# Performance work log

Hardware: AMD Instinct MI355X
Metric: run time of the kernel (lower is better)

## Reference

```python
import jax, jax.numpy as jnp
import numpy as np

N = 131072   # total nodes (B*C)
D = 128      # hidden_dim
H = 4        # gat_heads == hgt_heads
HD = 32      # head dim
T = 3        # number of edge types
E = 262144   # edges per edge type
B = 512      # graphs
EPS = 1e-6
SLOPE = 0.2  # LeakyReLU negative slope (module-wide and GAT internal)


def _rmsnorm(x, scale):
    return scale * x * jax.lax.rsqrt(jnp.mean(x * x, axis=-1, keepdims=True) + EPS)


def _gat(x, ei, W, a_src, a_dst, b):
    """HeteroConv(sum) of per-edge-type GATConv (concat heads, self-loops)."""
    loops = jnp.arange(N)

    def one(ei_t, W_t, as_t, ad_t):
        h = (x @ W_t).reshape(N, H, HD)                         # [N,H,HD]
        src = jnp.concatenate([ei_t[0], loops])                 # add self loops
        dst = jnp.concatenate([ei_t[1], loops])
        a = jax.nn.leaky_relu((h * as_t).sum(-1)[src] + (h * ad_t).sum(-1)[dst], SLOPE)  # [E',H]
        m = jax.ops.segment_max(a, dst, num_segments=N)
        ex = jnp.exp(a - m[dst])
        s = jax.ops.segment_sum(ex, dst, num_segments=N)
        alpha = ex / s[dst]                                     # segment softmax per dst
        out = jax.ops.segment_sum(h[src] * alpha[..., None], dst, num_segments=N)
        return out.reshape(N, D)

    return jax.vmap(one)(ei, W, a_src, a_dst).sum(0) + b.sum(0)


def _hgt(x, ei, kw, kb, qw, qb, vw, vb, rel_k, rel_v, rel_p, aw, ab, skip):
    """HGTConv, single node type, T edge types; softmax over all incoming edges."""
    k = (x @ kw + kb).reshape(N, H, HD)
    q = (x @ qw + qb).reshape(N, H, HD)
    v = (x @ vw + vb).reshape(N, H, HD)
    kt = jnp.einsum('nhd,thde->tnhe', k, rel_k)                 # relation-specific keys
    vt = jnp.einsum('nhd,thde->tnhe', v, rel_v)
    k_msg = jax.vmap(lambda a, i: a[i])(kt, ei[:, 0]).reshape(T * E, H, HD)
    v_msg = jax.vmap(lambda a, i: a[i])(vt, ei[:, 0]).reshape(T * E, H, HD)
    dst = ei[:, 1].reshape(T * E)
    p = jnp.broadcast_to(rel_p[:, None, :], (T, E, H)).reshape(T * E, H)
    score = (q[dst] * k_msg).sum(-1) * p / np.sqrt(HD)          # [T*E,H]
    m = jax.ops.segment_max(score, dst, num_segments=N)
    ex = jnp.exp(score - m[dst])
    s = jax.ops.segment_sum(ex, dst, num_segments=N)
    alpha = ex / s[dst]
    out = jax.ops.segment_sum(alpha[..., None] * v_msg, dst, num_segments=N).reshape(N, D)
    out = jax.nn.gelu(out, approximate=False) @ aw + ab
    g = jax.nn.sigmoid(skip)
    return g * out + (1.0 - g) * x


def _res(x_old, x_new, scale):
    # norm -> (dropout is identity in eval) -> residual -> LeakyReLU(0.2)
    return jax.nn.leaky_relu(x_old + _rmsnorm(x_new, scale), SLOPE)


def setup_inputs() -> dict:
    key = jax.random.key(0)
    ks = iter(jax.random.split(key, 48))

    def nrm(shape, std=0.1):
        return jax.random.normal(next(ks), shape, jnp.float32) * std

    inp = {}
    inp['x_cell'] = nrm((N, D), 1.0)
    inp['x_cell_embedded'] = nrm((N, D), 1.0)
    inp['z_h'] = nrm((B, D), 1.0)
    inp['edge_index'] = jax.random.randint(next(ks), (T, 2, E), 0, N)
    for l in ('gat1', 'gat2'):
        inp[l + '_w'] = nrm((T, D, H * HD))
        inp[l + '_att_src'] = nrm((T, H, HD))
        inp[l + '_att_dst'] = nrm((T, H, HD))
        inp[l + '_b'] = jnp.zeros((T, D), jnp.float32)
    inp['norm1_s'] = jnp.ones((D,), jnp.float32)
    inp['norm2_s'] = jnp.ones((D,), jnp.float32)
    inp['norm3_s'] = jnp.ones((D,), jnp.float32)
    for nm in ('k', 'q', 'v'):
        inp['hgt_%s_w' % nm] = nrm((D, D))
        inp['hgt_%s_b' % nm] = jnp.zeros((D,), jnp.float32)
    inp['hgt_rel_k'] = nrm((T, H, HD, HD))
    inp['hgt_rel_v'] = nrm((T, H, HD, HD))
    inp['hgt_rel_p'] = jnp.ones((T, H), jnp.float32)
    inp['hgt_a_w'] = nrm((D, D))
    inp['hgt_a_b'] = jnp.zeros((D,), jnp.float32)
    inp['hgt_skip'] = jnp.ones((), jnp.float32)
    inp['inj_w'] = nrm((D, D))
    inp['inj_b'] = jnp.zeros((D,), jnp.float32)
    inp['film_w1'] = nrm((D, 2 * D))
    inp['film_b1'] = jnp.zeros((2 * D,), jnp.float32)
    inp['film_w2'] = nrm((2 * D, 2 * D), 0.001)
    inp['film_b2'] = jnp.zeros((2 * D,), jnp.float32)
    inp['batch_size'] = B
    return inp


def reference(x_cell, x_cell_embedded, z_h, edge_index,
              gat1_w, gat1_att_src, gat1_att_dst, gat1_b,
              gat2_w, gat2_att_src, gat2_att_dst, gat2_b,
              norm1_s, norm2_s, norm3_s,
              hgt_k_w, hgt_k_b, hgt_q_w, hgt_q_b, hgt_v_w, hgt_v_b,
              hgt_rel_k, hgt_rel_v, hgt_rel_p, hgt_a_w, hgt_a_b, hgt_skip,
              inj_w, inj_b, film_w1, film_b1, film_w2, film_b2, batch_size):
    x1 = _res(x_cell, _gat(x_cell, edge_index, gat1_w, gat1_att_src, gat1_att_dst, gat1_b), norm1_s)
    x2 = _res(x1, _gat(x1, edge_index, gat2_w, gat2_att_src, gat2_att_dst, gat2_b), norm2_s)
    x3 = _res(x2, _hgt(x2, edge_index, hgt_k_w, hgt_k_b, hgt_q_w, hgt_q_b, hgt_v_w, hgt_v_b,
                       hgt_rel_k, hgt_rel_v, hgt_rel_p, hgt_a_w, hgt_a_b, hgt_skip), norm3_s)
    x3 = x3 + x_cell_embedded @ inj_w + inj_b                   # input injection
    # FiLM (per-graph z, fixed batch mode)
    gb = jax.nn.gelu(z_h @ film_w1 + film_b1, approximate=False) @ film_w2 + film_b2
    gamma, beta = jnp.split(gb, 2, axis=-1)
    gamma = 0.1 * jnp.tanh(gamma)
    beta = 0.1 * jnp.tanh(beta)
    C = N // batch_size
    out = (1.0 + gamma)[:, None, :] * x3.reshape(batch_size, C, D) + beta[:, None, :]
    return out.reshape(N, D)
```

## Files before the change

### kernel.cpp

```cpp
#include <hip/hip_runtime.h>
#include <math.h>
#include <cstdint>

#define NN     131072
#define DDIM   128
#define NHEAD  4
#define HDIM   32
#define NTYPE  3
#define NEDGE  262144
#define NGRAPH 512
#define EPSV   1e-6f
#define SLOPEV 0.2f

typedef unsigned short bfraw;
typedef __attribute__((ext_vector_type(8))) short bf16x8;
typedef __attribute__((ext_vector_type(4))) float f32x4;

__device__ __forceinline__ float lrelu(float x){ return x >= 0.f ? x : SLOPEV*x; }
__device__ __forceinline__ float gelu_f(float x){ return 0.5f*x*(1.f+erff(x*0.70710678118654752f)); }
__device__ __forceinline__ bfraw f2bf(float f){
  unsigned int u = __float_as_uint(f);
  u += 0x7fffu + ((u >> 16) & 1u);
  return (bfraw)(u >> 16);
}
__device__ __forceinline__ float4 ld_bf4(const bfraw* p){
  uint2 u = *reinterpret_cast<const uint2*>(p);
  float4 r;
  r.x = __uint_as_float(u.x << 16); r.y = __uint_as_float(u.x & 0xffff0000u);
  r.z = __uint_as_float(u.y << 16); r.w = __uint_as_float(u.y & 0xffff0000u);
  return r;
}
__device__ __forceinline__ bf16x8 pack_bf8(const float* p){
  float4 u = *reinterpret_cast<const float4*>(p);
  float4 v = *reinterpret_cast<const float4*>(p+4);
  bf16x8 r;
  r[0]=(short)f2bf(u.x); r[1]=(short)f2bf(u.y); r[2]=(short)f2bf(u.z); r[3]=(short)f2bf(u.w);
  r[4]=(short)f2bf(v.x); r[5]=(short)f2bf(v.y); r[6]=(short)f2bf(v.z); r[7]=(short)f2bf(v.w);
  return r;
}

__global__ void fill_k(float* __restrict__ p, float v, int n){
  int i = blockIdx.x*blockDim.x + threadIdx.x;
  int stride = gridDim.x*blockDim.x;
  for (; i < n; i += stride) p[i] = v;
}

__global__ void conv_k(const float* __restrict__ in, bfraw* __restrict__ out, int n){
  int i = blockIdx.x*blockDim.x + threadIdx.x;
  int stride = gridDim.x*blockDim.x;
  for (; i < n; i += stride) out[i] = f2bf(in[i]);
}

__global__ void hist_k(const int* __restrict__ ei, int* __restrict__ deg){
  int idx = blockIdx.x*256 + threadIdx.x;
  int t = idx >> 18, e = idx & (NEDGE-1);
  int d = ei[(long)t*2*NEDGE + NEDGE + e];
  atomicAdd(&deg[t*NN + d], 1);
}

__global__ void scan_a_k(const int* __restrict__ deg, int* __restrict__ rp,
                         int* __restrict__ csum){
  __shared__ int sh[256];
  int t = blockIdx.y, chunk = blockIdx.x, tid = threadIdx.x;
  const int* dp = deg + (long)t*NN + chunk*2048 + tid*8;
  int v[8]; int s = 0;
  #pragma unroll
  for (int i=0;i<8;i++){ v[i] = dp[i]; s += v[i]; }
  sh[tid] = s; __syncthreads();
  for (int off=1; off<256; off<<=1){
    int x = (tid>=off) ? sh[tid-off] : 0;
    __syncthreads();
    sh[tid] += x;
    __syncthreads();
  }
  int run = sh[tid] - s;
  int* op = rp + (long)t*(NN+1) + chunk*2048 + tid*8;
  #pragma unroll
  for (int i=0;i<8;i++){ op[i] = run; run += v[i]; }
  if (tid == 255) csum[t*64 + chunk] = sh[255];
}

__global__ void scan_b_k(int* __restrict__ csum){
  __shared__ int sh[64];
  int t = blockIdx.x, tid = threadIdx.x;
  int s = csum[t*64 + tid];
  sh[tid] = s; __syncthreads();
  for (int off=1; off<64; off<<=1){
    int x = (tid>=off) ? sh[tid-off] : 0;
    __syncthreads();
    sh[tid] += x;
    __syncthreads();
  }
  csum[t*64 + tid] = sh[tid] - s;
}

__global__ void scan_c_k(int* __restrict__ rp, const int* __restrict__ csum){
  int t = blockIdx.y, chunk = blockIdx.x, tid = threadIdx.x;
  int add = csum[t*64 + chunk];
  int* op = rp + (long)t*(NN+1) + chunk*2048 + tid*8;
  #pragma unroll
  for (int i=0;i<8;i++) op[i] += add;
  if (chunk == 63 && tid == 255) rp[(long)t*(NN+1) + NN] = NEDGE;
}

__global__ void scatter_k(const int* __restrict__ ei, const int* __restrict__ rp,
                          int* __restrict__ cnt, int* __restrict__ srcs){
  int idx = blockIdx.x*256 + threadIdx.x;
  int t = idx >> 18, e = idx & (NEDGE-1);
  int s = ei[(long)t*2*NEDGE + e];
  int d = ei[(long)t*2*NEDGE + NEDGE + e];
  int pos = rp[(long)t*(NN+1) + d] + atomicAdd(&cnt[t*NN + d], 1);
  srcs[(long)t*NEDGE + pos] = s;
}

__global__ void wswz_k(const float* g0a, const float* g0b, const float* g0c,
                       const float* g1a, const float* g1b, const float* g1c,
                       const float* qw,
                       const float* wk, const float* wv,
                       const float* aw, const float* injw,
                       bfraw* __restrict__ Wall)
{
  int y = blockIdx.y;
  const float* src;
  switch(y){
    case 0: src = g0a; break;  case 1: src = g0b; break;  case 2: src = g0c; break;
    case 3: src = g1a; break;  case 4: src = g1b; break;  case 5: src = g1c; break;
    case 6: src = qw; break;
    case 7: case 8: case 9: src = wk + (long)(y-7)*16384; break;
    case 10: case 11: case 12: src = wv + (long)(y-10)*16384; break;
    case 13: src = aw; break;
    default: src = injw; break;
  }
  int i = blockIdx.x*256 + threadIdx.x;
  int j = i & 7, lane = (i>>3) & 63, kc = (i>>9) & 3, nt = i >> 11;
  int k = kc*32 + ((lane>>4)<<3) + j;
  int n = nt*16 + (lane & 15);
  Wall[(long)y*16384 + i] = f2bf(src[k*DDIM + n]);
}

__global__ void gatproj_k(const float* __restrict__ w, const float* __restrict__ asrc,
                          const float* __restrict__ adst, bfraw* __restrict__ out)
{
  int i = blockIdx.x*256 + threadIdx.x;
  int j = i & 7, lane = (i>>3) & 63, kc = (i>>9) & 3, nt = i >> 11;
  int k = kc*32 + ((lane>>4)<<3) + j;
  int n = nt*16 + (lane & 15);
  float s = 0.f;
  if (n < 24){
    int t = n >> 3, sd = (n >> 2) & 1, hh = n & 3;
    const float* a  = (sd ? adst : asrc) + ((long)t*NHEAD + hh)*HDIM;
    const float* wr = w + ((long)t*DDIM + k)*DDIM + hh*HDIM;
    #pragma unroll 8
    for (int dd=0; dd<HDIM; dd++) s += wr[dd]*a[dd];
  }
  out[i] = f2bf(s);
}

__device__ __forceinline__ void load_afrags_bf16(const bfraw* __restrict__ A,
    long blockRow, int tid, bf16x8 a0[4], bf16x8 a1[4])
{
  const int w = tid >> 6, lane = tid & 63;
  const long rowA = blockRow + w*32 + (lane & 15);
  const bfraw* A0 = A + rowA*DDIM + ((lane>>4)<<3);
  #pragma unroll
  for (int kc=0;kc<4;kc++){
    a0[kc] = *reinterpret_cast<const bf16x8*>(A0 + kc*32);
    a1[kc] = *reinterpret_cast<const bf16x8*>(A0 + 16*DDIM + kc*32);
  }
}

__device__ __forceinline__ void load_afrags_f32(const float* __restrict__ A,
    long blockRow, int tid, bf16x8 a0[4], bf16x8 a1[4])
{
  const int w = tid >> 6, lane = tid & 63;
  const long rowA = blockRow + w*32 + (lane & 15);
  const float* A0 = A + rowA*DDIM + ((lane>>4)<<3);
  #pragma unroll
  for (int kc=0;kc<4;kc++){
    a0[kc] = pack_bf8(A0 + kc*32);
    a1[kc] = pack_bf8(A0 + 16*DDIM + kc*32);
  }
}

__device__ __forceinline__ void mfma_128(const bfraw* Wl, int lane,
    bf16x8 a0[4], bf16x8 a1[4], f32x4 acc0[8], f32x4 acc1[8])
{
  const f32x4 zz = {0.f,0.f,0.f,0.f};
  #pragma unroll
  for (int nt=0;nt<8;nt++){ acc0[nt]=zz; acc1[nt]=zz; }
  #pragma unroll
  for (int nt=0;nt<8;nt++){
    #pragma unroll
    for (int kc=0;kc<4;kc++){
      bf16x8 b = *reinterpret_cast<const bf16x8*>(Wl + ((nt*4+kc)*64 + lane)*8);
      acc0[nt] = __builtin_amdgcn_mfma_f32_16x16x32_bf16(a0[kc], b, acc0[nt], 0, 0, 0);
      acc1[nt] = __builtin_amdgcn_mfma_f32_16x16x32_bf16(a1[kc], b, acc1[nt], 0, 0, 0);
    }
  }
}

__device__ __forceinline__ void gemm_store_bf16(f32x4 acc0[8], f32x4 acc1[8],
    const float* bias, bfraw* __restrict__ Cb, long blockRow, int tid)
{
  const int w = tid>>6, lane = tid&63, q = lane>>4;
  #pragma unroll
  for (int g=0; g<2; g++){
    #pragma unroll
    for (int nt=0;nt<8;nt++){
      int col = nt*16 + (lane & 15);
      float bv = bias ? bias[col] : 0.f;
      #pragma unroll
      for (int r=0;r<4;r++){
        long row = blockRow + w*32 + g*16 + q*4 + r;
        float v = (g ? acc1[nt][r] : acc0[nt][r]) + bv;
        Cb[row*DDIM + col] = f2bf(v);
      }
    }
  }
}

__global__ __launch_bounds__(256) void gemm_out_k(
    const bfraw* __restrict__ A, const bfraw* __restrict__ Wsw,
    const float* __restrict__ bias, bfraw* __restrict__ Cb)
{
  __shared__ bfraw Wl[16384];
  const int tid = threadIdx.x;
  const long blockRow = (long)blockIdx.x * 128;
  #pragma unroll
  for (int i=0;i<8;i++)
    *reinterpret_cast<uint4*>(Wl + (i*256+tid)*8) =
        *reinterpret_cast<const uint4*>(Wsw + (i*256+tid)*8);
  __syncthreads();
  bf16x8 a0[4], a1[4];
  load_afrags_bf16(A, blockRow, tid, a0, a1);
  f32x4 acc0[8], acc1[8];
  mfma_128(Wl, tid & 63, a0, a1, acc0, acc1);
  gemm_store_bf16(acc0, acc1, bias, Cb, blockRow, tid);
}

__global__ __launch_bounds__(256) void gemm3_k(
    const bfraw* __restrict__ A,
    const bfraw* __restrict__ W0, const bfraw* __restrict__ W1,
    const bfraw* __restrict__ W2,
    const float* __restrict__ b0, const float* __restrict__ b1,
    const float* __restrict__ b2,
    bfraw* __restrict__ O0, bfraw* __restrict__ O1, bfraw* __restrict__ O2,
    const bfraw* __restrict__ Psw, float* __restrict__ SS)
{
  __shared__ bfraw Wl[16384];
  const int tid = threadIdx.x;
  const long blockRow = (long)blockIdx.x * 128;
  const int w = tid >> 6, lane = tid & 63;
  bf16x8 a0[4], a1[4];
  load_afrags_bf16(A, blockRow, tid, a0, a1);
  const bfraw* Ws[3] = {W0, W1, W2};
  const float* bs[3] = {b0, b1, b2};
  bfraw* Os[3] = {O0, O1, O2};
  #pragma unroll
  for (int t=0;t<3;t++){
    __syncthreads();
    #pragma unroll
    for (int i=0;i<8;i++)
      *reinterpret_cast<uint4*>(Wl + (i*256+tid)*8) =
          *reinterpret_cast<const uint4*>(Ws[t] + (i*256+tid)*8);
    __syncthreads();
    f32x4 acc0[8], acc1[8];
    mfma_128(Wl, lane, a0, a1, acc0, acc1);
    gemm_store_bf16(acc0, acc1, bs[t], Os[t], blockRow, tid);
  }
  if (Psw){
    __syncthreads();
    #pragma unroll
    for (int i=0;i<2;i++)
      *reinterpret_cast<uint4*>(Wl + (i*256+tid)*8) =
          *reinterpret_cast<const uint4*>(Psw + (i*256+tid)*8);
    __syncthreads();
    const f32x4 zz = {0.f,0.f,0.f,0.f};
    f32x4 acc0[2], acc1[2];
    #pragma unroll
    for (int nt=0;nt<2;nt++){ acc0[nt]=zz; acc1[nt]=zz; }
    #pragma unroll
    for (int nt=0;nt<2;nt++){
      #pragma unroll
      for (int kc=0;kc<4;kc++){
        bf16x8 b = *reinterpret_cast<const bf16x8*>(Wl + ((nt*4+kc)*64 + lane)*8);
        acc0[nt] = __builtin_amdgcn_mfma_f32_16x16x32_bf16(a0[kc], b, acc0[nt], 0, 0, 0);
        acc1[nt] = __builtin_amdgcn_mfma_f32_16x16x32_bf16(a1[kc], b, acc1[nt], 0, 0, 0);
      }
    }
    const int q = lane >> 4;
    #pragma unroll
    for (int g=0; g<2; g++){
      #pragma unroll
      for (int nt=0;nt<2;nt++){
        int col = nt*16 + (lane & 15);
        if (col < 24){
          int tt = col >> 3, c = col & 7;
          #pragma unroll
          for (int r=0;r<4;r++){
            long row = blockRow + w*32 + g*16 + q*4 + r;
            SS[(((long)tt*NN + row)<<3) + c] = (g ? acc1[nt][r] : acc0[nt][r]);
          }
        }
      }
    }
  }
}

__global__ __launch_bounds__(256) void gemm_res3_k(
    const bfraw* __restrict__ A, const bfraw* __restrict__ Wsw,
    const float* __restrict__ bias, float* __restrict__ X,
    const float* __restrict__ norm, const float* __restrict__ skip)
{
  __shared__ bfraw Wl[16384];
  const int tid = threadIdx.x;
  const long blockRow = (long)blockIdx.x * 128;
  #pragma unroll
  for (int i=0;i<8;i++)
    *reinterpret_cast<uint4*>(Wl + (i*256+tid)*8) =
        *reinterpret_cast<const uint4*>(Wsw + (i*256+tid)*8);
  __syncthreads();
  bf16x8 a0[4], a1[4];
  load_afrags_bf16(A, blockRow, tid, a0, a1);
  f32x4 acc0[8], acc1[8];
  mfma_128(Wl, tid & 63, a0, a1, acc0, acc1);
  const int w = tid>>6, lane = tid&63, q = lane>>4;
  const float gsk = 1.f/(1.f + __expf(-skip[0]));
  #pragma unroll
  for (int g=0; g<2; g++){
    #pragma unroll
    for (int r=0;r<4;r++){
      long row = blockRow + w*32 + g*16 + q*4 + r;
      float vv[8], xx[8];
      float sq = 0.f;
      #pragma unroll
      for (int nt=0;nt<8;nt++){
        int col = nt*16 + (lane & 15);
        float o  = (g ? acc1[nt][r] : acc0[nt][r]) + bias[col];
        float xo = X[row*DDIM + col];
        float v  = gsk*o + (1.f-gsk)*xo;
        vv[nt] = v; xx[nt] = xo; sq += v*v;
      }
      sq += __shfl_xor(sq, 1, 64);
      sq += __shfl_xor(sq, 2, 64);
      sq += __shfl_xor(sq, 4, 64);
      sq += __shfl_xor(sq, 8, 64);
      float rr = rsqrtf(sq*(1.f/DDIM) + EPSV);
      #pragma unroll
      for (int nt=0;nt<8;nt++){
        int col = nt*16 + (lane & 15);
        X[row*DDIM + col] = lrelu(xx[nt] + norm[col]*vv[nt]*rr);
      }
    }
  }
}

__global__ __launch_bounds__(256) void gemm_film_k(
    const float* __restrict__ Af, const bfraw* __restrict__ Wsw,
    const float* __restrict__ bias, const float* __restrict__ Xadd,
    const float* __restrict__ gbt, float* __restrict__ out)
{
  __shared__ bfraw Wl[16384];
  const int tid = threadIdx.x;
  const long blockRow = (long)blockIdx.x * 128;
  #pragma unroll
  for (int i=0;i<8;i++)
    *reinterpret_cast<uint4*>(Wl + (i*256+tid)*8) =
        *reinterpret_cast<const uint4*>(Wsw + (i*256+tid)*8);
  __syncthreads();
  bf16x8 a0[4], a1[4];
  load_afrags_f32(Af, blockRow, tid, a0, a1);
  f32x4 acc0[8], acc1[8];
  mfma_128(Wl, tid & 63, a0, a1, acc0, acc1);
  const int w = tid>>6, lane = tid&63, q = lane>>4;
  #pragma unroll
  for (int g=0; g<2; g++){
    #pragma unroll
    for (int nt=0;nt<8;nt++){
      int col = nt*16 + (lane & 15);
      float bv = bias[col];
      #pragma unroll
      for (int r=0;r<4;r++){
        long row = blockRow + w*32 + g*16 + q*4 + r;
        long gi  = row >> 8;
        float v  = (g ? acc1[nt][r] : acc0[nt][r]) + bv + Xadd[row*DDIM + col];
        float ga = gbt[gi*256 + col];
        float be = gbt[gi*256 + 128 + col];
        out[row*DDIM + col] = (1.f + ga)*v + be;
      }
    }
  }
}

__global__ __launch_bounds__(256) void gat_fused_k(
    const int* __restrict__ rp, const int* __restrict__ srcs,
    const bfraw* __restrict__ H0, const bfraw* __restrict__ H1,
    const bfraw* __restrict__ H2, const float* __restrict__ SS,
    const float* __restrict__ gatb, const float* __restrict__ xold,
    const float* __restrict__ norm, float* __restrict__ X, bfraw* __restrict__ Xb)
{
  int node = blockIdx.x*8 + (threadIdx.x >> 5);
  int l = threadIdx.x & 31;
  int hd = l >> 3;
  const bfraw* Hs[3] = {H0, H1, H2};
  float tx=0.f, ty=0.f, tz=0.f, tw=0.f;
  #pragma unroll
  for (int t=0; t<3; t++){
    const bfraw* Ht = Hs[t];
    const float* St = SS + ((long)t*NN)*8;
    float dsv = St[(long)node*8 + 4 + hd];
    float e = __expf(lrelu(St[(long)node*8 + hd] + dsv));
    float lsum = e;
    float4 a4 = ld_bf4(Ht + (long)node*DDIM + l*4);
    a4.x *= e; a4.y *= e; a4.z *= e; a4.w *= e;
    int beg = rp[t*(NN+1) + node], end = rp[t*(NN+1) + node + 1];
    const int* sp = srcs + (long)t*NEDGE;
    for (int p=beg; p<end; p++){
      int s = sp[p];
      float ee = __expf(lrelu(St[(long)s*8 + hd] + dsv));
      float4 hv = ld_bf4(Ht + (long)s*DDIM + l*4);
      lsum += ee;
      a4.x += ee*hv.x; a4.y += ee*hv.y; a4.z += ee*hv.z; a4.w += ee*hv.w;
    }
    float inv = 1.f/lsum;
    tx += a4.x*inv; ty += a4.y*inv; tz += a4.z*inv; tw += a4.w*inv;
  }
  int f = l*4;
  tx += gatb[f]   + gatb[DDIM+f]   + gatb[2*DDIM+f];
  ty += gatb[f+1] + gatb[DDIM+f+1] + gatb[2*DDIM+f+1];
  tz += gatb[f+2] + gatb[DDIM+f+2] + gatb[2*DDIM+f+2];
  tw += gatb[f+3] + gatb[DDIM+f+3] + gatb[2*DDIM+f+3];
  float sq = tx*tx + ty*ty + tz*tz + tw*tw;
  sq += __shfl_xor(sq, 1, 64);
  sq += __shfl_xor(sq, 2, 64);
  sq += __shfl_xor(sq, 4, 64);
  sq += __shfl_xor(sq, 8, 64);
  sq += __shfl_xor(sq, 16, 64);
  float r = rsqrtf(sq*(1.f/DDIM) + EPSV);
  float4 x4 = *reinterpret_cast<const float4*>(xold + (long)node*DDIM + f);
  float4 o;
  o.x = lrelu(x4.x + norm[f]  *tx*r);
  o.y = lrelu(x4.y + norm[f+1]*ty*r);
  o.z = lrelu(x4.z + norm[f+2]*tz*r);
  o.w = lrelu(x4.w + norm[f+3]*tw*r);
  *reinterpret_cast<float4*>(X + (long)node*DDIM + f) = o;
  unsigned int lo = ((unsigned int)f2bf(o.y) << 16) | f2bf(o.x);
  unsigned int hi = ((unsigned int)f2bf(o.w) << 16) | f2bf(o.z);
  *reinterpret_cast<uint2*>(Xb + (long)node*DDIM + f) = make_uint2(lo, hi);
}

__global__ void fold_k(const float* __restrict__ w, const float* __restrict__ b,
                       const float* __restrict__ rel, float* __restrict__ Weff,
                       float* __restrict__ beff)
{
  int idx = blockIdx.x*256 + threadIdx.x;
  if (idx >= NTYPE*DDIM*DDIM) return;
  int he = idx & 127, c = (idx >> 7) & 127, t = idx >> 14;
  int h = he >> 5, e = he & 31;
  const float* wrow = w + (long)c*DDIM + h*HDIM;
  const float* relm = rel + ((long)(t*NHEAD + h)*HDIM)*HDIM + e;
  float s = 0.f;
  #pragma unroll 8
  for (int d=0; d<HDIM; d++) s += wrow[d] * relm[d*HDIM];
  Weff[(long)t*DDIM*DDIM + (long)c*DDIM + he] = s;
  if (c == 0){
    float sb = 0.f;
    #pragma unroll 8
    for (int d=0; d<HDIM; d++) sb += b[h*HDIM+d] * relm[d*HDIM];
    beff[(long)t*DDIM + he] = sb;
  }
}

__global__ __launch_bounds__(256) void hgt_score_pass_k(
    const int* __restrict__ rp, const int* __restrict__ srcs,
    const bfraw* __restrict__ qb, const bfraw* __restrict__ kt,
    const float* __restrict__ relp, float* __restrict__ E)
{
  int node = blockIdx.x*8 + (threadIdx.x >> 5);
  int l = threadIdx.x & 31;
  int hd = l >> 3, sub = l & 7;
  float4 qv = ld_bf4(qb + (long)node*DDIM + l*4);
  int beg = rp[node], end = rp[node+1];
  float scale = relp[hd] * 0.17677669529663687f;
  for (int p=beg; p<end; p++){
    int s = srcs[p];
    float4 kv = ld_bf4(kt + (long)s*DDIM + l*4);
    float dot = qv.x*kv.x + qv.y*kv.y + qv.z*kv.z + qv.w*kv.w;
    dot += __shfl_xor(dot, 1, 64);
    dot += __shfl_xor(dot, 2, 64);
    dot += __shfl_xor(dot, 4, 64);
    if (sub == 0) E[(long)p*4 + hd] = __expf(dot * scale);
  }
}

__global__ __launch_bounds__(256) void hgt_acc_fused_k(
    const int* __restrict__ rp, const int* __restrict__ srcs,
    const float* __restrict__ E, const bfraw* __restrict__ V0,
    const bfraw* __restrict__ V1, const bfraw* __restrict__ V2,
    bfraw* __restrict__ out)
{
  int node = blockIdx.x*8 + (threadIdx.x >> 5);
  int l = threadIdx.x & 31;
  int hd = l >> 3;
  float ax=0.f, ay=0.f, az=0.f, aw=0.f, lsum=0.f;
  const bfraw* Vs[3] = {V0, V1, V2};
  #pragma unroll
  for (int t=0; t<3; t++){
    const bfraw* Vt = Vs[t];
    const float* Ep = E + (long)t*NEDGE*4;
    const int* sp = srcs + (long)t*NEDGE;
    int beg = rp[t*(NN+1) + node], end = rp[t*(NN+1) + node + 1];
    for (int p=beg; p<end; p++){
      int s = sp[p];
      float ex = Ep[(long)p*4 + hd];
      float4 vv = ld_bf4(Vt + (long)s*DDIM + l*4);
      ax += ex*vv.x; ay += ex*vv.y; az += ex*vv.z; aw += ex*vv.w;
      lsum += ex;
    }
  }
  float inv = (lsum > 0.f) ? 1.f/lsum : 0.f;
  float o0 = gelu_f(ax*inv), o1 = gelu_f(ay*inv);
  float o2 = gelu_f(az*inv), o3 = gelu_f(aw*inv);
  unsigned int lo = ((unsigned int)f2bf(o1) << 16) | f2bf(o0);
  unsigned int hi = ((unsigned int)f2bf(o3) << 16) | f2bf(o2);
  *reinterpret_cast<uint2*>(out + (long)node*DDIM + l*4) = make_uint2(lo, hi);
}

__global__ void film1_k(const float* __restrict__ z, const float* __restrict__ w1,
                        const float* __restrict__ b1, float* __restrict__ f1)
{
  int idx = blockIdx.x*256 + threadIdx.x;
  if (idx >= NGRAPH*256) return;
  int j = idx & 255, b = idx >> 8;
  const float* zr = z + (long)b*DDIM;
  float s = b1[j];
  for (int k=0;k<DDIM;k++) s += zr[k] * w1[(long)k*256 + j];
  f1[idx] = gelu_f(s);
}

__global__ void film2_k(const float* __restrict__ f1, const float* __restrict__ w2,
                        const float* __restrict__ b2, float* __restrict__ gb)
{
  int idx = blockIdx.x*256 + threadIdx.x;
  if (idx >= NGRAPH*256) return;
  int j = idx & 255, b = idx >> 8;
  const float* fr = f1 + (long)b*256;
  float s = b2[j];
  for (int k=0;k<256;k++) s += fr[k] * w2[(long)k*256 + j];
  gb[idx] = 0.1f*tanhf(s);
}

extern "C" void kernel_launch(void* const* d_in, const int* in_sizes, int n_in,
                              void* d_out, int out_size, void* d_ws, size_t ws_size,
                              hipStream_t stream)
{
  (void)in_sizes; (void)n_in; (void)out_size; (void)ws_size;
  const float* x_cell = (const float*)d_in[0];
  const float* x_emb  = (const float*)d_in[1];
  const float* z_h    = (const float*)d_in[2];
  const int*   ei     = (const int*)d_in[3];
  const float* gw[2]  = {(const float*)d_in[4],  (const float*)d_in[8]};
  const float* gas[2] = {(const float*)d_in[5],  (const float*)d_in[9]};
  const float* gad[2] = {(const float*)d_in[6],  (const float*)d_in[10]};
  const float* gbi[2] = {(const float*)d_in[7],  (const float*)d_in[11]};
  const float* norm1  = (const float*)d_in[12];
  const float* norm2  = (const float*)d_in[13];
  const float* norm3  = (const float*)d_in[14];
  const float* kw = (const float*)d_in[15]; const float* kb = (const float*)d_in[16];
  const float* qw = (const float*)d_in[17]; const float* qb = (const float*)d_in[18];
  const float* vw = (const float*)d_in[19]; const float* vb = (const float*)d_in[20];
  const float* relk = (const float*)d_in[21];
  const float* relv = (const float*)d_in[22];
  const float* relp = (const float*)d_in[23];
  const float* aw = (const float*)d_in[24]; const float* ab = (const float*)d_in[25];
  const float* skip = (const float*)d_in[26];
  const float* injw = (const float*)d_in[27]; const float* injb = (const float*)d_in[28];
  const float* fw1 = (const float*)d_in[29]; const float* fb1 = (const float*)d_in[30];
  const float* fw2 = (const float*)d_in[31]; const float* fb2 = (const float*)d_in[32];

  const long ND = (long)NN*DDIM;
  float* X    = (float*)d_ws;
  float* K    = X + ND;
  bfraw* Xb   = (bfraw*)(K + ND);
  bfraw* Hb   = Xb + ND;
  float* Sbuf = (float*)(Hb + ND);
  float* sA   = Sbuf + (long)NTYPE*NEDGE*4;
  float* sB   = sA + (long)NN*4;
  float* WkE  = sB + (long)NN*4;
  float* bkE  = WkE + (long)NTYPE*DDIM*DDIM;
  float* WvE  = bkE + (long)NTYPE*DDIM;
  float* bvE  = WvE + (long)NTYPE*DDIM*DDIM;
  bfraw* Pswz = (bfraw*)(bvE + (long)NTYPE*DDIM);
  bfraw* Wall = Pswz + (long)2*4096;
  float* f1b  = (float*)(Wall + (long)15*16384);
  float* gbb  = f1b + (long)NGRAPH*256;
  int*   deg  = (int*)(gbb + (long)NGRAPH*256);
  int*   rp   = deg + (long)NTYPE*NN;
  int*   srcs = rp  + (long)NTYPE*(NN+1);
  int*   csum = srcs + (long)NTYPE*NEDGE;

  bfraw* Kb0 = (bfraw*)K;
  bfraw* Kb1 = Kb0 + ND;

  const dim3 b256(256);
  float* NF = nullptr;
  bfraw* NB = nullptr; (void)NB;

  fill_k<<<256, b256, 0, stream>>>((float*)deg, 0.f, NTYPE*NN);
  hist_k<<<(NTYPE*NEDGE)/256, b256, 0, stream>>>(ei, deg);
  scan_a_k<<<dim3(64, NTYPE), b256, 0, stream>>>(deg, rp, csum);
  scan_b_k<<<NTYPE, 64, 0, stream>>>(csum);
  scan_c_k<<<dim3(64, NTYPE), b256, 0, stream>>>(rp, csum);
  fill_k<<<256, b256, 0, stream>>>((float*)deg, 0.f, NTYPE*NN);
  scatter_k<<<(NTYPE*NEDGE)/256, b256, 0, stream>>>(ei, rp, deg, srcs);

  fold_k<<<(NTYPE*DDIM*DDIM)/256, b256, 0, stream>>>(kw, kb, relk, WkE, bkE);
  fold_k<<<(NTYPE*DDIM*DDIM)/256, b256, 0, stream>>>(vw, vb, relv, WvE, bvE);
  wswz_k<<<dim3(64, 15), b256, 0, stream>>>(
      gw[0], gw[0]+16384, gw[0]+32768,
      gw[1], gw[1]+16384, gw[1]+32768,
      qw, WkE, WvE, aw, injw, Wall);
  gatproj_k<<<16, b256, 0, stream>>>(gw[0], gas[0], gad[0], Pswz);
  gatproj_k<<<16, b256, 0, stream>>>(gw[1], gas[1], gad[1], Pswz + 4096);

  film1_k<<<(NGRAPH*256)/256, b256, 0, stream>>>(z_h, fw1, fb1, f1b);
  film2_k<<<(NGRAPH*256)/256, b256, 0, stream>>>(f1b, fw2, fb2, gbb);

  conv_k<<<2048, b256, 0, stream>>>(x_cell, Xb, (int)ND);
  for (int layer=0; layer<2; layer++){
    gemm3_k<<<NN/128, b256, 0, stream>>>(
        Xb,
        Wall + (long)(layer*3+0)*16384, Wall + (long)(layer*3+1)*16384,
        Wall + (long)(layer*3+2)*16384,
        NF, NF, NF,
        Hb, Kb0, Kb1,
        Pswz + (long)layer*4096, Sbuf);
    gat_fused_k<<<NN/8, b256, 0, stream>>>(
        rp, srcs, Hb, Kb0, Kb1, Sbuf, gbi[layer],
        (layer==0) ? x_cell : X, (layer==0) ? norm1 : norm2, X, Xb);
  }

  gemm3_k<<<NN/128, b256, 0, stream>>>(
      Xb, Wall + (long)6*16384, Wall + (long)7*16384, Wall + (long)8*16384,
      qb, bkE, bkE + DDIM,
      Kb0, Hb, Kb1, nullptr, nullptr);
  hgt_score_pass_k<<<NN/8, b256, 0, stream>>>(rp, srcs, Kb0, Hb, relp, Sbuf);
  hgt_score_pass_k<<<NN/8, b256, 0, stream>>>(rp + (NN+1), srcs + NEDGE, Kb0, Kb1,
      relp + NHEAD, Sbuf + (long)NEDGE*4);
  gemm_out_k<<<NN/128, b256, 0, stream>>>(Xb, Wall + (long)9*16384, bkE + 2*DDIM, Hb);
  hgt_score_pass_k<<<NN/8, b256, 0, stream>>>(rp + 2*(NN+1), srcs + 2*NEDGE, Kb0, Hb,
      relp + 2*NHEAD, Sbuf + (long)2*NEDGE*4);
  gemm3_k<<<NN/128, b256, 0, stream>>>(
      Xb, Wall + (long)10*16384, Wall + (long)11*16384, Wall + (long)12*16384,
      bvE, bvE + DDIM, bvE + 2*DDIM,
      Hb, Kb0, Kb1, nullptr, nullptr);
  hgt_acc_fused_k<<<NN/8, b256, 0, stream>>>(rp, srcs, Sbuf, Hb, Kb0, Kb1, Xb);
  gemm_res3_k<<<NN/128, b256, 0, stream>>>(Xb, Wall + (long)13*16384, ab,
                                           X, norm3, skip);
  gemm_film_k<<<NN/128, b256, 0, stream>>>(x_emb, Wall + (long)14*16384, injb,
                                           X, gbb, (float*)d_out);
}
```

Measured before the change: 962.6 us.

## Fuse conversion, HGT output+FiLM, score passes; fold rel_p scale; unroll edge loops

```diff
diff --git a/kernel.cpp b/kernel.cpp
--- a/kernel.cpp
+++ b/kernel.cpp
@@ -43,12 +43,6 @@
   int i = blockIdx.x*blockDim.x + threadIdx.x;
   int stride = gridDim.x*blockDim.x;
   for (; i < n; i += stride) p[i] = v;
-}
-
-__global__ void conv_k(const float* __restrict__ in, bfraw* __restrict__ out, int n){
-  int i = blockIdx.x*blockDim.x + threadIdx.x;
-  int stride = gridDim.x*blockDim.x;
-  for (; i < n; i += stride) out[i] = f2bf(in[i]);
 }
 
 __global__ void hist_k(const int* __restrict__ ei, int* __restrict__ deg){
@@ -239,7 +233,7 @@
 }
 
 __global__ __launch_bounds__(256) void gemm3_k(
-    const bfraw* __restrict__ A,
+    const bfraw* __restrict__ Ab, const float* __restrict__ Af,
     const bfraw* __restrict__ W0, const bfraw* __restrict__ W1,
     const bfraw* __restrict__ W2,
     const float* __restrict__ b0, const float* __restrict__ b1,
@@ -252,7 +246,8 @@
   const long blockRow = (long)blockIdx.x * 128;
   const int w = tid >> 6, lane = tid & 63;
   bf16x8 a0[4], a1[4];
-  load_afrags_bf16(A, blockRow, tid, a0, a1);
+  if (Af) load_afrags_f32(Af, blockRow, tid, a0, a1);
+  else    load_afrags_bf16(Ab, blockRow, tid, a0, a1);
   const bfraw* Ws[3] = {W0, W1, W2};
   const float* bs[3] = {b0, b1, b2};
   bfraw* Os[3] = {O0, O1, O2};
@@ -307,10 +302,13 @@
   }
 }
 
-__global__ __launch_bounds__(256) void gemm_res3_k(
-    const bfraw* __restrict__ A, const bfraw* __restrict__ Wsw,
-    const float* __restrict__ bias, float* __restrict__ X,
-    const float* __restrict__ norm, const float* __restrict__ skip)
+__global__ __launch_bounds__(256) void gemm_r3film_k(
+    const bfraw* __restrict__ Aattn, const bfraw* __restrict__ Waw,
+    const float* __restrict__ ab, const float* __restrict__ X,
+    const float* __restrict__ norm, const float* __restrict__ skip,
+    const float* __restrict__ xemb, const bfraw* __restrict__ Winj,
+    const float* __restrict__ injb, const float* __restrict__ gbt,
+    float* __restrict__ out)
 {
   __shared__ bfraw Wl[16384];
   const int tid = threadIdx.x;
@@ -318,12 +316,21 @@
   #pragma unroll
   for (int i=0;i<8;i++)
     *reinterpret_cast<uint4*>(Wl + (i*256+tid)*8) =
-        *reinterpret_cast<const uint4*>(Wsw + (i*256+tid)*8);
+        *reinterpret_cast<const uint4*>(Waw + (i*256+tid)*8);
   __syncthreads();
   bf16x8 a0[4], a1[4];
-  load_afrags_bf16(A, blockRow, tid, a0, a1);
-  f32x4 acc0[8], acc1[8];
-  mfma_128(Wl, tid & 63, a0, a1, acc0, acc1);
+  load_afrags_bf16(Aattn, blockRow, tid, a0, a1);
+  f32x4 accA0[8], accA1[8];
+  mfma_128(Wl, tid & 63, a0, a1, accA0, accA1);
+  __syncthreads();
+  #pragma unroll
+  for (int i=0;i<8;i++)
+    *reinterpret_cast<uint4*>(Wl + (i*256+tid)*8) =
+        *reinterpret_cast<const uint4*>(Winj + (i*256+tid)*8);
+  __syncthreads();
+  load_afrags_f32(xemb, blockRow, tid, a0, a1);
+  f32x4 accB0[8], accB1[8];
+  mfma_128(Wl, tid & 63, a0, a1, accB0, accB1);
   const int w = tid>>6, lane = tid&63, q = lane>>4;
   const float gsk = 1.f/(1.f + __expf(-skip[0]));
   #pragma unroll
@@ -336,9 +343,9 @@
       #pragma unroll
       for (int nt=0;nt<8;nt++){
         int col = nt*16 + (lane & 15);
-        float o  = (g ? acc1[nt][r] : acc0[nt][r]) + bias[col];
+        float oA = (g ? accA1[nt][r] : accA0[nt][r]) + ab[col];
         float xo = X[row*DDIM + col];
-        float v  = gsk*o + (1.f-gsk)*xo;
+        float v  = gsk*oA + (1.f-gsk)*xo;
         vv[nt] = v; xx[nt] = xo; sq += v*v;
       }
       sq += __shfl_xor(sq, 1, 64);
@@ -346,47 +353,13 @@
       sq += __shfl_xor(sq, 4, 64);
       sq += __shfl_xor(sq, 8, 64);
       float rr = rsqrtf(sq*(1.f/DDIM) + EPSV);
+      long gi = row >> 8;
       #pragma unroll
       for (int nt=0;nt<8;nt++){
         int col = nt*16 + (lane & 15);
-        X[row*DDIM + col] = lrelu(xx[nt] + norm[col]*vv[nt]*rr);
-      }
-    }
-  }
-}
-
-__global__ __launch_bounds__(256) void gemm_film_k(
-    const float* __restrict__ Af, const bfraw* __restrict__ Wsw,
-    const float* __restrict__ bias, const float* __restrict__ Xadd,
-    const float* __restrict__ gbt, float* __restrict__ out)
-{
-  __shared__ bfraw Wl[16384];
-  const int tid = threadIdx.x;
-  const long blockRow = (long)blockIdx.x * 128;
-  #pragma unroll
-  for (int i=0;i<8;i++)
-    *reinterpret_cast<uint4*>(Wl + (i*256+tid)*8) =
-        *reinterpret_cast<const uint4*>(Wsw + (i*256+tid)*8);
-  __syncthreads();
-  bf16x8 a0[4], a1[4];
-  load_afrags_f32(Af, blockRow, tid, a0, a1);
-  f32x4 acc0[8], acc1[8];
-  mfma_128(Wl, tid & 63, a0, a1, acc0, acc1);
-  const int w = tid>>6, lane = tid&63, q = lane>>4;
-  #pragma unroll
-  for (int g=0; g<2; g++){
-    #pragma unroll
-    for (int nt=0;nt<8;nt++){
-      int col = nt*16 + (lane & 15);
-      float bv = bias[col];
-      #pragma unroll
-      for (int r=0;r<4;r++){
-        long row = blockRow + w*32 + g*16 + q*4 + r;
-        long gi  = row >> 8;
-        float v  = (g ? acc1[nt][r] : acc0[nt][r]) + bv + Xadd[row*DDIM + col];
-        float ga = gbt[gi*256 + col];
-        float be = gbt[gi*256 + 128 + col];
-        out[row*DDIM + col] = (1.f + ga)*v + be;
+        float x3 = lrelu(xx[nt] + norm[col]*vv[nt]*rr);
+        float vB = (g ? accB1[nt][r] : accB0[nt][r]) + injb[col] + x3;
+        out[row*DDIM + col] = (1.f + gbt[gi*256 + col])*vB + gbt[gi*256 + 128 + col];
       }
     }
   }
@@ -403,27 +376,50 @@
   int l = threadIdx.x & 31;
   int hd = l >> 3;
   const bfraw* Hs[3] = {H0, H1, H2};
+  float dsv[3], ssl[3]; float4 hsl[3]; int beg[3], end[3];
+  #pragma unroll
+  for (int t=0; t<3; t++){
+    const float* St = SS + ((long)t*NN)*8;
+    dsv[t] = St[(long)node*8 + 4 + hd];
+    ssl[t] = St[(long)node*8 + hd];
+    hsl[t] = ld_bf4(Hs[t] + (long)node*DDIM + l*4);
+    beg[t] = rp[t*(NN+1) + node];
+    end[t] = rp[t*(NN+1) + node + 1];
+  }
   float tx=0.f, ty=0.f, tz=0.f, tw=0.f;
   #pragma unroll
   for (int t=0; t<3; t++){
     const bfraw* Ht = Hs[t];
     const float* St = SS + ((long)t*NN)*8;
-    float dsv = St[(long)node*8 + 4 + hd];
-    float e = __expf(lrelu(St[(long)node*8 + hd] + dsv));
-    float lsum = e;
-    float4 a4 = ld_bf4(Ht + (long)node*DDIM + l*4);
-    a4.x *= e; a4.y *= e; a4.z *= e; a4.w *= e;
-    int beg = rp[t*(NN+1) + node], end = rp[t*(NN+1) + node + 1];
     const int* sp = srcs + (long)t*NEDGE;
-    for (int p=beg; p<end; p++){
-      int s = sp[p];
-      float ee = __expf(lrelu(St[(long)s*8 + hd] + dsv));
-      float4 hv = ld_bf4(Ht + (long)s*DDIM + l*4);
-      lsum += ee;
-      a4.x += ee*hv.x; a4.y += ee*hv.y; a4.z += ee*hv.z; a4.w += ee*hv.w;
-    }
-    float inv = 1.f/lsum;
-    tx += a4.x*inv; ty += a4.y*inv; tz += a4.z*inv; tw += a4.w*inv;
+    const float d = dsv[t];
+    float e = __expf(lrelu(ssl[t] + d));
+    float lA = e, lB = 0.f;
+    float4 aA = make_float4(e*hsl[t].x, e*hsl[t].y, e*hsl[t].z, e*hsl[t].w);
+    float4 aB = make_float4(0.f,0.f,0.f,0.f);
+    int p = beg[t];
+    for (; p+1 < end[t]; p += 2){
+      int s0 = sp[p], s1 = sp[p+1];
+      float v0 = St[(long)s0*8 + hd];
+      float v1 = St[(long)s1*8 + hd];
+      float4 h0 = ld_bf4(Ht + (long)s0*DDIM + l*4);
+      float4 h1 = ld_bf4(Ht + (long)s1*DDIM + l*4);
+      float e0 = __expf(lrelu(v0 + d));
+      float e1 = __expf(lrelu(v1 + d));
+      lA += e0; lB += e1;
+      aA.x += e0*h0.x; aA.y += e0*h0.y; aA.z += e0*h0.z; aA.w += e0*h0.w;
+      aB.x += e1*h1.x; aB.y += e1*h1.y; aB.z += e1*h1.z; aB.w += e1*h1.w;
+    }
+    if (p < end[t]){
+      int s0 = sp[p];
+      float e0 = __expf(lrelu(St[(long)s0*8 + hd] + d));
+      float4 h0 = ld_bf4(Ht + (long)s0*DDIM + l*4);
+      lA += e0;
+      aA.x += e0*h0.x; aA.y += e0*h0.y; aA.z += e0*h0.z; aA.w += e0*h0.w;
+    }
+    float inv = 1.f/(lA + lB);
+    tx += (aA.x+aB.x)*inv; ty += (aA.y+aB.y)*inv;
+    tz += (aA.z+aB.z)*inv; tw += (aA.w+aB.w)*inv;
   }
   int f = l*4;
   tx += gatb[f]   + gatb[DDIM+f]   + gatb[2*DDIM+f];
@@ -450,46 +446,103 @@
 }
 
 __global__ void fold_k(const float* __restrict__ w, const float* __restrict__ b,
-                       const float* __restrict__ rel, float* __restrict__ Weff,
-                       float* __restrict__ beff)
+                       const float* __restrict__ rel, const float* __restrict__ scl,
+                       float* __restrict__ Weff, float* __restrict__ beff)
 {
   int idx = blockIdx.x*256 + threadIdx.x;
   if (idx >= NTYPE*DDIM*DDIM) return;
   int he = idx & 127, c = (idx >> 7) & 127, t = idx >> 14;
   int h = he >> 5, e = he & 31;
+  float fs = scl ? scl[t*NHEAD + h]*0.17677669529663687f : 1.f;
   const float* wrow = w + (long)c*DDIM + h*HDIM;
   const float* relm = rel + ((long)(t*NHEAD + h)*HDIM)*HDIM + e;
   float s = 0.f;
   #pragma unroll 8
   for (int d=0; d<HDIM; d++) s += wrow[d] * relm[d*HDIM];
-  Weff[(long)t*DDIM*DDIM + (long)c*DDIM + he] = s;
+  Weff[(long)t*DDIM*DDIM + (long)c*DDIM + he] = s*fs;
   if (c == 0){
     float sb = 0.f;
     #pragma unroll 8
     for (int d=0; d<HDIM; d++) sb += b[h*HDIM+d] * relm[d*HDIM];
-    beff[(long)t*DDIM + he] = sb;
-  }
-}
-
-__global__ __launch_bounds__(256) void hgt_score_pass_k(
+    beff[(long)t*DDIM + he] = sb*fs;
+  }
+}
+
+__global__ __launch_bounds__(256) void hgt_score2_k(
+    const int* __restrict__ rp, const int* __restrict__ srcs,
+    const bfraw* __restrict__ qb, const bfraw* __restrict__ kt0,
+    const bfraw* __restrict__ kt1, float* __restrict__ E)
+{
+  int node = blockIdx.x*8 + (threadIdx.x >> 5);
+  int l = threadIdx.x & 31;
+  int hd = l >> 3, sub = l & 7;
+  float4 qv = ld_bf4(qb + (long)node*DDIM + l*4);
+  #pragma unroll
+  for (int t=0; t<2; t++){
+    const bfraw* kt = t ? kt1 : kt0;
+    const int* sp = srcs + (long)t*NEDGE;
+    float* Et = E + (long)t*NEDGE*4;
+    int beg = rp[t*(NN+1) + node], end = rp[t*(NN+1) + node + 1];
+    int p = beg;
+    for (; p+1 < end; p += 2){
+      int s0 = sp[p], s1 = sp[p+1];
+      float4 k0 = ld_bf4(kt + (long)s0*DDIM + l*4);
+      float4 k1 = ld_bf4(kt + (long)s1*DDIM + l*4);
+      float d0 = qv.x*k0.x + qv.y*k0.y + qv.z*k0.z + qv.w*k0.w;
+      float d1 = qv.x*k1.x + qv.y*k1.y + qv.z*k1.z + qv.w*k1.w;
+      d0 += __shfl_xor(d0, 1, 64);  d1 += __shfl_xor(d1, 1, 64);
+      d0 += __shfl_xor(d0, 2, 64);  d1 += __shfl_xor(d1, 2, 64);
+      d0 += __shfl_xor(d0, 4, 64);  d1 += __shfl_xor(d1, 4, 64);
+      if (sub == 0){
+        Et[(long)p*4 + hd]     = __expf(d0);
+        Et[(long)(p+1)*4 + hd] = __expf(d1);
+      }
+    }
+    if (p < end){
+      int s0 = sp[p];
+      float4 k0 = ld_bf4(kt + (long)s0*DDIM + l*4);
+      float d0 = qv.x*k0.x + qv.y*k0.y + qv.z*k0.z + qv.w*k0.w;
+      d0 += __shfl_xor(d0, 1, 64);
+      d0 += __shfl_xor(d0, 2, 64);
+      d0 += __shfl_xor(d0, 4, 64);
+      if (sub == 0) Et[(long)p*4 + hd] = __expf(d0);
+    }
+  }
+}
+
+__global__ __launch_bounds__(256) void hgt_score1_k(
     const int* __restrict__ rp, const int* __restrict__ srcs,
     const bfraw* __restrict__ qb, const bfraw* __restrict__ kt,
-    const float* __restrict__ relp, float* __restrict__ E)
+    float* __restrict__ E)
 {
   int node = blockIdx.x*8 + (threadIdx.x >> 5);
   int l = threadIdx.x & 31;
   int hd = l >> 3, sub = l & 7;
   float4 qv = ld_bf4(qb + (long)node*DDIM + l*4);
   int beg = rp[node], end = rp[node+1];
-  float scale = relp[hd] * 0.17677669529663687f;
-  for (int p=beg; p<end; p++){
-    int s = srcs[p];
-    float4 kv = ld_bf4(kt + (long)s*DDIM + l*4);
-    float dot = qv.x*kv.x + qv.y*kv.y + qv.z*kv.z + qv.w*kv.w;
-    dot += __shfl_xor(dot, 1, 64);
-    dot += __shfl_xor(dot, 2, 64);
-    dot += __shfl_xor(dot, 4, 64);
-    if (sub == 0) E[(long)p*4 + hd] = __expf(dot * scale);
+  int p = beg;
+  for (; p+1 < end; p += 2){
+    int s0 = srcs[p], s1 = srcs[p+1];
+    float4 k0 = ld_bf4(kt + (long)s0*DDIM + l*4);
+    float4 k1 = ld_bf4(kt + (long)s1*DDIM + l*4);
+    float d0 = qv.x*k0.x + qv.y*k0.y + qv.z*k0.z + qv.w*k0.w;
+    float d1 = qv.x*k1.x + qv.y*k1.y + qv.z*k1.z + qv.w*k1.w;
+    d0 += __shfl_xor(d0, 1, 64);  d1 += __shfl_xor(d1, 1, 64);
+    d0 += __shfl_xor(d0, 2, 64);  d1 += __shfl_xor(d1, 2, 64);
+    d0 += __shfl_xor(d0, 4, 64);  d1 += __shfl_xor(d1, 4, 64);
+    if (sub == 0){
+      E[(long)p*4 + hd]     = __expf(d0);
+      E[(long)(p+1)*4 + hd] = __expf(d1);
+    }
+  }
+  if (p < end){
+    int s0 = srcs[p];
+    float4 k0 = ld_bf4(kt + (long)s0*DDIM + l*4);
+    float d0 = qv.x*k0.x + qv.y*k0.y + qv.z*k0.z + qv.w*k0.w;
+    d0 += __shfl_xor(d0, 1, 64);
+    d0 += __shfl_xor(d0, 2, 64);
+    d0 += __shfl_xor(d0, 4, 64);
+    if (sub == 0) E[(long)p*4 + hd] = __expf(d0);
   }
 }
 
@@ -502,7 +555,8 @@
   int node = blockIdx.x*8 + (threadIdx.x >> 5);
   int l = threadIdx.x & 31;
   int hd = l >> 3;
-  float ax=0.f, ay=0.f, az=0.f, aw=0.f, lsum=0.f;
+  float axA=0.f, ayA=0.f, azA=0.f, awA=0.f, lsA=0.f;
+  float axB=0.f, ayB=0.f, azB=0.f, awB=0.f, lsB=0.f;
   const bfraw* Vs[3] = {V0, V1, V2};
   #pragma unroll
   for (int t=0; t<3; t++){
@@ -510,17 +564,27 @@
     const float* Ep = E + (long)t*NEDGE*4;
     const int* sp = srcs + (long)t*NEDGE;
     int beg = rp[t*(NN+1) + node], end = rp[t*(NN+1) + node + 1];
-    for (int p=beg; p<end; p++){
-      int s = sp[p];
-      float ex = Ep[(long)p*4 + hd];
-      float4 vv = ld_bf4(Vt + (long)s*DDIM + l*4);
-      ax += ex*vv.x; ay += ex*vv.y; az += ex*vv.z; aw += ex*vv.w;
-      lsum += ex;
-    }
-  }
+    int p = beg;
+    for (; p+1 < end; p += 2){
+      int s0 = sp[p], s1 = sp[p+1];
+      float e0 = Ep[(long)p*4 + hd];
+      float e1 = Ep[(long)(p+1)*4 + hd];
+      float4 v0 = ld_bf4(Vt + (long)s0*DDIM + l*4);
+      float4 v1 = ld_bf4(Vt + (long)s1*DDIM + l*4);
+      axA += e0*v0.x; ayA += e0*v0.y; azA += e0*v0.z; awA += e0*v0.w; lsA += e0;
+      axB += e1*v1.x; ayB += e1*v1.y; azB += e1*v1.z; awB += e1*v1.w; lsB += e1;
+    }
+    if (p < end){
+      int s0 = sp[p];
+      float e0 = Ep[(long)p*4 + hd];
+      float4 v0 = ld_bf4(Vt + (long)s0*DDIM + l*4);
+      axA += e0*v0.x; ayA += e0*v0.y; azA += e0*v0.z; awA += e0*v0.w; lsA += e0;
+    }
+  }
+  float lsum = lsA + lsB;
   float inv = (lsum > 0.f) ? 1.f/lsum : 0.f;
-  float o0 = gelu_f(ax*inv), o1 = gelu_f(ay*inv);
-  float o2 = gelu_f(az*inv), o3 = gelu_f(aw*inv);
+  float o0 = gelu_f((axA+axB)*inv), o1 = gelu_f((ayA+ayB)*inv);
+  float o2 = gelu_f((azA+azB)*inv), o3 = gelu_f((awA+awB)*inv);
   unsigned int lo = ((unsigned int)f2bf(o1) << 16) | f2bf(o0);
   unsigned int hi = ((unsigned int)f2bf(o3) << 16) | f2bf(o2);
   *reinterpret_cast<uint2*>(out + (long)node*DDIM + l*4) = make_uint2(lo, hi);
@@ -604,7 +668,7 @@
 
   const dim3 b256(256);
   float* NF = nullptr;
-  bfraw* NB = nullptr; (void)NB;
+  bfraw* NB = nullptr; (void)NB; (void)sA; (void)sB;
 
   fill_k<<<256, b256, 0, stream>>>((float*)deg, 0.f, NTYPE*NN);
   hist_k<<<(NTYPE*NEDGE)/256, b256, 0, stream>>>(ei, deg);
@@ -614,8 +678,8 @@
   fill_k<<<256, b256, 0, stream>>>((float*)deg, 0.f, NTYPE*NN);
   scatter_k<<<(NTYPE*NEDGE)/256, b256, 0, stream>>>(ei, rp, deg, srcs);
 
-  fold_k<<<(NTYPE*DDIM*DDIM)/256, b256, 0, stream>>>(kw, kb, relk, WkE, bkE);
-  fold_k<<<(NTYPE*DDIM*DDIM)/256, b256, 0, stream>>>(vw, vb, relv, WvE, bvE);
+  fold_k<<<(NTYPE*DDIM*DDIM)/256, b256, 0, stream>>>(kw, kb, relk, relp, WkE, bkE);
+  fold_k<<<(NTYPE*DDIM*DDIM)/256, b256, 0, stream>>>(vw, vb, relv, NF, WvE, bvE);
   wswz_k<<<dim3(64, 15), b256, 0, stream>>>(
       gw[0], gw[0]+16384, gw[0]+32768,
       gw[1], gw[1]+16384, gw[1]+32768,
@@ -626,10 +690,9 @@
   film1_k<<<(NGRAPH*256)/256, b256, 0, stream>>>(z_h, fw1, fb1, f1b);
   film2_k<<<(NGRAPH*256)/256, b256, 0, stream>>>(f1b, fw2, fb2, gbb);
 
-  conv_k<<<2048, b256, 0, stream>>>(x_cell, Xb, (int)ND);
   for (int layer=0; layer<2; layer++){
     gemm3_k<<<NN/128, b256, 0, stream>>>(
-        Xb,
+        Xb, (layer==0) ? x_cell : NF,
         Wall + (long)(layer*3+0)*16384, Wall + (long)(layer*3+1)*16384,
         Wall + (long)(layer*3+2)*16384,
         NF, NF, NF,
@@ -641,22 +704,19 @@
   }
 
   gemm3_k<<<NN/128, b256, 0, stream>>>(
-      Xb, Wall + (long)6*16384, Wall + (long)7*16384, Wall + (long)8*16384,
+      Xb, NF, Wall + (long)6*16384, Wall + (long)7*16384, Wall + (long)8*16384,
       qb, bkE, bkE + DDIM,
       Kb0, Hb, Kb1, nullptr, nullptr);
-  hgt_score_pass_k<<<NN/8, b256, 0, stream>>>(rp, srcs, Kb0, Hb, relp, Sbuf);
-  hgt_score_pass_k<<<NN/8, b256, 0, stream>>>(rp + (NN+1), srcs + NEDGE, Kb0, Kb1,
-      relp + NHEAD, Sbuf + (long)NEDGE*4);
+  hgt_score2_k<<<NN/8, b256, 0, stream>>>(rp, srcs, Kb0, Hb, Kb1, Sbuf);
   gemm_out_k<<<NN/128, b256, 0, stream>>>(Xb, Wall + (long)9*16384, bkE + 2*DDIM, Hb);
-  hgt_score_pass_k<<<NN/8, b256, 0, stream>>>(rp + 2*(NN+1), srcs + 2*NEDGE, Kb0, Hb,
-      relp + 2*NHEAD, Sbuf + (long)2*NEDGE*4);
+  hgt_score1_k<<<NN/8, b256, 0, stream>>>(rp + 2*(NN+1), srcs + 2*NEDGE, Kb0, Hb,
+      Sbuf + (long)2*NEDGE*4);
   gemm3_k<<<NN/128, b256, 0, stream>>>(
-      Xb, Wall + (long)10*16384, Wall + (long)11*16384, Wall + (long)12*16384,
+      Xb, NF, Wall + (long)10*16384, Wall + (long)11*16384, Wall + (long)12*16384,
       bvE, bvE + DDIM, bvE + 2*DDIM,
       Hb, Kb0, Kb1, nullptr, nullptr);
   hgt_acc_fused_k<<<NN/8, b256, 0, stream>>>(rp, srcs, Sbuf, Hb, Kb0, Kb1, Xb);
-  gemm_res3_k<<<NN/128, b256, 0, stream>>>(Xb, Wall + (long)13*16384, ab,
-                                           X, norm3, skip);
-  gemm_film_k<<<NN/128, b256, 0, stream>>>(x_emb, Wall + (long)14*16384, injb,
-                                           X, gbb, (float*)d_out);
-}
+  gemm_r3film_k<<<NN/128, b256, 0, stream>>>(
+      Xb, Wall + (long)13*16384, ab, X, norm3, skip,
+      x_emb, Wall + (long)14*16384, injb, gbb, (float*)d_out);
+}
```

Result: faster. 878.1 us (-8.8%).
